# Kernel optimization log

Hardware: AMD Instinct MI355X
Metric: run time of the kernel (lower is better)

Reference implementation:

```python
import jax, jax.numpy as jnp
import numpy as np


def setup_inputs() -> dict:
    key = jax.random.key(0)
    C, S, NQ, H = 10, 10, 30, 1024  # n_classes, n_support, n_query, h_dim
    ks = jax.random.split(key, 6)
    x = jax.random.normal(ks[0], (C * (S + NQ), H), dtype=jnp.float32)
    # sorted, balanced labels so y.eq(c).nonzero() picks contiguous blocks
    y = jnp.repeat(jnp.arange(C, dtype=jnp.int32), S + NQ)
    W1 = jax.random.normal(ks[1], (H, H), dtype=jnp.float32) / np.sqrt(H)
    b1 = jnp.zeros((H,), dtype=jnp.float32)
    W2 = jax.random.normal(ks[2], (4 * H, H), dtype=jnp.float32) / np.sqrt(4 * H)
    b2 = jnp.zeros((H,), dtype=jnp.float32)
    return {"x": x, "W1": W1, "b1": b1, "W2": W2, "b2": b2,
            "y": y, "n_classes": C, "n_support": S, "n_query": NQ, "flag": 0}


def reference(x, W1, b1, W2, b2, y, n_classes, n_support, n_query, flag):
    # flag == 0 path; y is sorted & balanced, so the label-based gather in the
    # original (y.eq(c).nonzero()[:S] / [S:]) reduces to a reshape.
    C, S, NQ = n_classes, n_support, n_query
    H = x.shape[-1]
    xr = x.reshape(C, S + NQ, H)
    support = xr[:, :S]                      # [C, S, H]
    query = xr[:, S:].reshape(C * NQ, H)     # [Qt, H], Qt = C*NQ

    # fc1 computed ONCE on support/query, then broadcast (same math as
    # applying fc1 to the expanded tensors in the original).
    sf = jnp.einsum('csh,hd->csd', support, W1) + b1   # [C, S, H]
    qf = query @ W1 + b1                               # [Qt, H]

    # fc2 on concat([sf, qf, |sf-qf|, sf*qf]) split into 4 blocks of W2 so we
    # never materialize the [Qt, C, S, 4H] concat.
    Ws, Wq, Wc, Wd = W2[:H], W2[H:2 * H], W2[2 * H:3 * H], W2[3 * H:]
    a_s = jnp.einsum('csh,hd->csd', sf, Ws)            # [C, S, H]
    a_q = qf @ Wq                                      # [Qt, H]
    sfb = sf[None]                                     # [1, C, S, H]
    qfb = qf[:, None, None]                            # [Qt, 1, 1, H]
    d1 = jnp.abs(sfb - qfb)                            # [Qt, C, S, H]
    d2 = sfb * qfb                                     # [Qt, C, S, H]
    mca_ = (a_s[None] + a_q[:, None, None]
            + jnp.einsum('qcsh,hd->qcsd', d1, Wc)
            + jnp.einsum('qcsh,hd->qcsd', d2, Wd) + b2)  # [Qt, C, S, H]

    score = jax.nn.softmax(jnp.tanh(mca_).sum(-1), axis=-1)  # [Qt, C, S]
    proto = jnp.einsum('qcs,csh->qch', score, support)       # [Qt, C, H]
    dists = jnp.sum((proto - query[:, None, :]) ** 2, axis=-1)  # [Qt, C]
    return dists
```

## Files before the change

kernel.cpp:

```cpp
#include <hip/hip_runtime.h>
#include <hip/hip_bf16.h>
#include <math.h>

#define C_   10
#define S_   10
#define NQ_  30
#define H_   1024
#define Q_   300
#define ROWS_ 400

typedef __attribute__((ext_vector_type(8))) short s16x8;
typedef __attribute__((ext_vector_type(4))) float f32x4;

static __device__ __forceinline__ short f2b(float f) {
  __hip_bfloat16 h = __float2bfloat16(f);
  return __builtin_bit_cast(short, h);
}

static __device__ __forceinline__ float ftanh(float v) {
  v = fminf(fmaxf(v, -10.f), 10.f);
  float e = __expf(2.f * v);
  return (e - 1.f) / (e + 1.f);
}

__global__ __launch_bounds__(256) void feat_kernel(
    const float* __restrict__ x, const float* __restrict__ W1,
    const float* __restrict__ b1, float* __restrict__ f) {
  __shared__ float xs[4][H_];
  const int rt = blockIdx.x % 100;
  const int nt = blockIdx.x / 100;
  const int r0 = rt * 4;
  const int n0 = nt * 256;
  const int tid = threadIdx.x;

  for (int t = tid; t < 4 * H_ / 4; t += 256) {
    int r = t >> 8, h4 = (t & 255) * 4;
    *(float4*)&xs[r][h4] = *(const float4*)&x[(size_t)(r0 + r) * H_ + h4];
  }
  __syncthreads();

  float acc0 = 0.f, acc1 = 0.f, acc2 = 0.f, acc3 = 0.f;
  const float* __restrict__ wp = W1 + n0 + tid;
#pragma unroll 8
  for (int h = 0; h < H_; ++h) {
    float w = wp[(size_t)h * H_];
    acc0 = fmaf(xs[0][h], w, acc0);
    acc1 = fmaf(xs[1][h], w, acc1);
    acc2 = fmaf(xs[2][h], w, acc2);
    acc3 = fmaf(xs[3][h], w, acc3);
  }
  const int col = n0 + tid;
  const float bb = b1[col];
  f[(size_t)(r0 + 0) * H_ + col] = acc0 + bb;
  f[(size_t)(r0 + 1) * H_ + col] = acc1 + bb;
  f[(size_t)(r0 + 2) * H_ + col] = acc2 + bb;
  f[(size_t)(r0 + 3) * H_ + col] = acc3 + bb;
}

__global__ __launch_bounds__(256) void proj_kernel(
    const float* __restrict__ f, const float* __restrict__ W2,
    const float* __restrict__ b2, float* __restrict__ a) {
  __shared__ float fs[4][H_];
  const int rt = blockIdx.x % 100;
  const int nt = blockIdx.x / 100;
  const bool isSup = (rt < 25);
  const int i0 = isSup ? rt * 4 : (rt - 25) * 4;
  const int n0 = nt * 256;
  const float* __restrict__ W = isSup ? W2 : (W2 + (size_t)H_ * H_);
  const int tid = threadIdx.x;

  for (int t = tid; t < 4 * H_ / 4; t += 256) {
    int r = t >> 8, h4 = (t & 255) * 4;
    int i = i0 + r;
    int row = isSup ? ((i / 10) * 40 + (i % 10)) : ((i / 30) * 40 + 10 + (i % 30));
    *(float4*)&fs[r][h4] = *(const float4*)&f[(size_t)row * H_ + h4];
  }
  __syncthreads();

  float acc0 = 0.f, acc1 = 0.f, acc2 = 0.f, acc3 = 0.f;
  const float* __restrict__ wp = W + n0 + tid;
#pragma unroll 8
  for (int h = 0; h < H_; ++h) {
    float w = wp[(size_t)h * H_];
    acc0 = fmaf(fs[0][h], w, acc0);
    acc1 = fmaf(fs[1][h], w, acc1);
    acc2 = fmaf(fs[2][h], w, acc2);
    acc3 = fmaf(fs[3][h], w, acc3);
  }
  const int col = n0 + tid;
  const float bb = isSup ? 0.f : b2[col];
  const int o0 = isSup ? i0 : (100 + i0);
  a[(size_t)(o0 + 0) * H_ + col] = acc0 + bb;
  a[(size_t)(o0 + 1) * H_ + col] = acc1 + bb;
  a[(size_t)(o0 + 2) * H_ + col] = acc2 + bb;
  a[(size_t)(o0 + 3) * H_ + col] = acc3 + bb;
}

__global__ __launch_bounds__(256) void trans_kernel(
    const float* __restrict__ W2, unsigned short* __restrict__ Bt,
    float* __restrict__ logits) {
  const int b = blockIdx.x;
  const int tid = threadIdx.x;
  if (b == 512) {
    float4* lz = (float4*)logits;
    for (int i = tid; i < 7500; i += 256) lz[i] = make_float4(0.f, 0.f, 0.f, 0.f);
    return;
  }
  const int mat = b >> 8, kt = (b >> 4) & 15, ntl = b & 15;
  const float* __restrict__ src =
      W2 + (size_t)(2 + mat) * H_ * H_ + (size_t)(kt * 64) * H_ + ntl * 64;
  __shared__ float tl[64][65];
  {
    int r = tid >> 2, c4 = (tid & 3) * 16;
    const float* srcp = src + (size_t)r * H_ + c4;
#pragma unroll
    for (int j = 0; j < 4; ++j) {
      float4 v = *(const float4*)(srcp + j * 4);
      tl[r][c4 + j * 4 + 0] = v.x;
      tl[r][c4 + j * 4 + 1] = v.y;
      tl[r][c4 + j * 4 + 2] = v.z;
      tl[r][c4 + j * 4 + 3] = v.w;
    }
  }
  __syncthreads();
  {
    int n = tid >> 2, k0t = (tid & 3) * 16;
    s16x8 o0, o1;
#pragma unroll
    for (int j = 0; j < 8; ++j) {
      o0[j] = f2b(tl[k0t + j][n]);
      o1[j] = f2b(tl[k0t + 8 + j][n]);
    }
    unsigned short* dstp = Bt + (size_t)mat * H_ * H_ +
                           (size_t)(ntl * 64 + n) * H_ + kt * 64 + k0t;
    *(s16x8*)dstp = o0;
    *(s16x8*)(dstp + 8) = o1;
  }
}

__global__ __launch_bounds__(256, 2) void mca_mfma_kernel(
    const float* __restrict__ f, const float* __restrict__ a,
    const unsigned short* __restrict__ Bt, float* __restrict__ logits) {
  const int b = blockIdx.x;
  const int nt = b & 7;
  const int qt = (b >> 3) % 19;
  const int c = (b >> 3) / 19;
  const int q0 = qt * 16;
  const int n0 = nt * 128;

  __shared__ unsigned short Als[2][160 * 64];
  __shared__ unsigned short Bls[2][128 * 64];
  __shared__ float sl[2][26][36];

  const int tid = threadIdx.x;
  const int w = tid >> 6, lane = tid & 63;

  const int str = tid >> 3, sseg = tid & 7;
  int sgrow;
  if (str < 10) sgrow = c * 40 + str;
  else {
    int qg = q0 + (str - 10);
    if (qg > 299) qg = 299;
    sgrow = (qg / 30) * 40 + 10 + (qg % 30);
  }
  const float* fb_stage = f + (size_t)sgrow * H_ + sseg * 4;
  const unsigned st_off = (unsigned)(str * 144 + sseg * 16);

  const int rbase = tid >> 2, qtr = tid & 3;
  const bool has2 = (tid < 128);
  unsigned sboff[3], qboff[3], awx[3], aw2x[3];
#pragma unroll
  for (int j = 0; j < 3; ++j) {
    int row = (j < 2) ? (rbase + j * 64) : (128 + rbase);
    int qloc = row / 10, s = row - qloc * 10;
    sboff[j] = (unsigned)(s * 144 + qtr * 32);
    qboff[j] = (unsigned)((10 + qloc) * 144 + qtr * 32);
    unsigned asw = (unsigned)((row & 7) << 4);
    unsigned aw = (unsigned)(row * 128 + qtr * 16);
    awx[j] = aw ^ asw;
    aw2x[j] = (aw + 64) ^ asw;
  }

  const int rlo = lane >> 3;
  const int cch = (lane & 7) ^ rlo;
  const unsigned short* bsrc[4];
  unsigned bldso[4];
#pragma unroll
  for (int i = 0; i < 4; ++i) {
    int row = w * 32 + i * 8 + rlo;
    bsrc[i] = Bt + (size_t)(cch >> 2) * H_ * H_ + (size_t)(n0 + row) * H_ +
              (cch & 3) * 8;
    bldso[i] = (unsigned)(w * 4096 + i * 1024);
  }

  const int frow = lane & 15;
  const unsigned fkb = (unsigned)((lane >> 4) * 16);
  const unsigned swf = (unsigned)((frow & 7) << 4);
  const int wr = w >> 1, wc = w & 1;
  unsigned ard[5], brd[4];
#pragma unroll
  for (int m = 0; m < 5; ++m) ard[m] = (unsigned)((wr * 80 + m * 16 + frow) * 128);
#pragma unroll
  for (int nf = 0; nf < 4; ++nf) brd[nf] = (unsigned)((wc * 64 + nf * 16 + frow) * 128);

  f32x4 acc[5][4];
#pragma unroll
  for (int m = 0; m < 5; ++m)
#pragma unroll
    for (int nf = 0; nf < 4; ++nf) acc[m][nf] = (f32x4)(0.f);

#define STAGE(SLP, KS)                                                         \
  do {                                                                         \
    if (tid < 208) {                                                           \
      float4 v = *(const float4*)(fb_stage + (KS) * 32);                       \
      *(float4*)((char*)&sl[SLP][0][0] + st_off) = v;                          \
    }                                                                          \
  } while (0)

#define DMA_B(P, KG)                                                           \
  do {                                                                         \
    _Pragma("unroll") for (int i = 0; i < 4; ++i) {                            \
      __builtin_amdgcn_global_load_lds(                                        \
          (const __attribute__((address_space(1))) unsigned int*)(bsrc[i] + (KG)), \
          (__attribute__((address_space(3))) unsigned int*)((char*)&Bls[P][0] + bldso[i]), \
          16, 0, 0);                                                           \
    }                                                                          \
  } while (0)

#define GTASK(J, SLB, AB)                                                      \
  do {                                                                         \
    float4 sa = *(const float4*)((SLB) + sboff[J]);                            \
    float4 sb2 = *(const float4*)((SLB) + sboff[J] + 16);                      \
    float4 qa = *(const float4*)((SLB) + qboff[J]);                            \
    float4 qb2 = *(const float4*)((SLB) + qboff[J] + 16);                      \
    s16x8 d1, d2;                                                              \
    d1[0] = f2b(fabsf(sa.x - qa.x)); d2[0] = f2b(sa.x * qa.x);                 \
    d1[1] = f2b(fabsf(sa.y - qa.y)); d2[1] = f2b(sa.y * qa.y);                 \
    d1[2] = f2b(fabsf(sa.z - qa.z)); d2[2] = f2b(sa.z * qa.z);                 \
    d1[3] = f2b(fabsf(sa.w - qa.w)); d2[3] = f2b(sa.w * qa.w);                 \
    d1[4] = f2b(fabsf(sb2.x - qb2.x)); d2[4] = f2b(sb2.x * qb2.x);             \
    d1[5] = f2b(fabsf(sb2.y - qb2.y)); d2[5] = f2b(sb2.y * qb2.y);             \
    d1[6] = f2b(fabsf(sb2.z - qb2.z)); d2[6] = f2b(sb2.z * qb2.z);             \
    d1[7] = f2b(fabsf(sb2.w - qb2.w)); d2[7] = f2b(sb2.w * qb2.w);             \
    *(s16x8*)((AB) + awx[J]) = d1;                                             \
    *(s16x8*)((AB) + aw2x[J]) = d2;                                            \
  } while (0)

#define GENX(SLP, ABP)                                                         \
  do {                                                                         \
    const char* SLB = (const char*)&sl[SLP][0][0];                             \
    char* AB = (char*)&Als[ABP][0];                                            \
    GTASK(0, SLB, AB);                                                         \
    GTASK(1, SLB, AB);                                                         \
    if (has2) GTASK(2, SLB, AB);                                               \
  } while (0)

#define MFMA_PHASE(P)                                                          \
  do {                                                                         \
    const char* AB = (const char*)&Als[P][0];                                  \
    const char* BB = (const char*)&Bls[P][0];                                  \
    _Pragma("unroll") for (int kk = 0; kk < 2; ++kk) {                         \
      const unsigned kb = fkb + kk * 64;                                       \
      s16x8 bf0 = *(const s16x8*)(BB + ((brd[0] + kb) ^ swf));                 \
      s16x8 bf1 = *(const s16x8*)(BB + ((brd[1] + kb) ^ swf));                 \
      s16x8 bf2 = *(const s16x8*)(BB + ((brd[2] + kb) ^ swf));                 \
      s16x8 bf3 = *(const s16x8*)(BB + ((brd[3] + kb) ^ swf));                 \
      _Pragma("unroll") for (int m = 0; m < 5; ++m) {                          \
        s16x8 af = *(const s16x8*)(AB + ((ard[m] + kb) ^ swf));                \
        acc[m][0] = __builtin_amdgcn_mfma_f32_16x16x32_bf16(af, bf0, acc[m][0], 0, 0, 0); \
        acc[m][1] = __builtin_amdgcn_mfma_f32_16x16x32_bf16(af, bf1, acc[m][1], 0, 0, 0); \
        acc[m][2] = __builtin_amdgcn_mfma_f32_16x16x32_bf16(af, bf2, acc[m][2], 0, 0, 0); \
        acc[m][3] = __builtin_amdgcn_mfma_f32_16x16x32_bf16(af, bf3, acc[m][3], 0, 0, 0); \
      }                                                                        \
    }                                                                          \
  } while (0)

  STAGE(0, 0);
  STAGE(1, 1);
  DMA_B(0, 0);
  __syncthreads();
  GENX(0, 0);
  __syncthreads();

  for (int kp = 0; kp < 16; ++kp) {
    const int ks = kp * 2;
    DMA_B(1, (ks + 1) * 32);
    GENX(1, 1);
    __builtin_amdgcn_s_setprio(1);
    MFMA_PHASE(0);
    __builtin_amdgcn_s_setprio(0);
    if (kp < 15) STAGE(0, ks + 2);
    __syncthreads();

    if (kp < 15) {
      DMA_B(0, (ks + 2) * 32);
      GENX(0, 0);
      __builtin_amdgcn_s_setprio(1);
      MFMA_PHASE(1);
      __builtin_amdgcn_s_setprio(0);
      STAGE(1, ks + 3);
      __syncthreads();
    } else {
      __builtin_amdgcn_s_setprio(1);
      MFMA_PHASE(1);
      __builtin_amdgcn_s_setprio(0);
    }
  }

  const int colb = n0 + wc * 64 + frow;
  const int rgrp = (lane >> 4) * 4;
#pragma unroll
  for (int m = 0; m < 5; ++m) {
#pragma unroll
    for (int r = 0; r < 4; ++r) {
      const int row = wr * 80 + m * 16 + rgrp + r;
      const int qloc = row / 10, s = row - qloc * 10;
      const int q = q0 + qloc;
      float t = 0.f;
#pragma unroll
      for (int nf = 0; nf < 4; ++nf) {
        const int col = colb + nf * 16;
        float v = acc[m][nf][r] + a[(size_t)(c * 10 + s) * H_ + col] +
                  a[(size_t)(100 + q) * H_ + col];
        t += ftanh(v);
      }
      t += __shfl_xor(t, 1);
      t += __shfl_xor(t, 2);
      t += __shfl_xor(t, 4);
      t += __shfl_xor(t, 8);
      if ((lane & 15) == 0 && q < 300)
        atomicAdd(&logits[(q * 10 + c) * 10 + s], t);
    }
  }
#undef STAGE
#undef DMA_B
#undef GTASK
#undef GENX
#undef MFMA_PHASE
}

__global__ __launch_bounds__(256) void out_kernel(
    const float* __restrict__ x, const float* __restrict__ logits,
    float* __restrict__ dists) {
  const int q = blockIdx.x / 10;
  const int c = blockIdx.x % 10;
  const int tid = threadIdx.x;
  const int lane = tid & 63;
  const int wave = tid >> 6;
  __shared__ float red[4];

  float l[S_];
  float m = -1e30f;
#pragma unroll
  for (int s = 0; s < S_; ++s) {
    l[s] = logits[(q * 10 + c) * 10 + s];
    m = fmaxf(m, l[s]);
  }
  float sum = 0.f;
  float sc[S_];
#pragma unroll
  for (int s = 0; s < S_; ++s) {
    sc[s] = __expf(l[s] - m);
    sum += sc[s];
  }
  float inv = 1.f / sum;
#pragma unroll
  for (int s = 0; s < S_; ++s) sc[s] *= inv;

  const int qr = (q / 30) * 40 + 10 + (q % 30);
  float part = 0.f;
#pragma unroll
  for (int ii = 0; ii < 4; ++ii) {
    int i = tid + ii * 256;
    float p = 0.f;
#pragma unroll
    for (int s = 0; s < S_; ++s)
      p = fmaf(sc[s], x[(size_t)(c * 40 + s) * H_ + i], p);
    float d = p - x[(size_t)qr * H_ + i];
    part = fmaf(d, d, part);
  }
  for (int off = 32; off; off >>= 1) part += __shfl_down(part, off);
  if (lane == 0) red[wave] = part;
  __syncthreads();
  if (tid == 0) dists[q * 10 + c] = red[0] + red[1] + red[2] + red[3];
}

extern "C" void kernel_launch(void* const* d_in, const int* in_sizes, int n_in,
                              void* d_out, int out_size, void* d_ws, size_t ws_size,
                              hipStream_t stream) {
  const float* x = (const float*)d_in[0];
  const float* W1 = (const float*)d_in[1];
  const float* b1 = (const float*)d_in[2];
  const float* W2 = (const float*)d_in[3];
  const float* b2 = (const float*)d_in[4];
  float* out = (float*)d_out;

  float* f = (float*)d_ws;
  float* a = f + ROWS_ * H_;
  float* logits = a + ROWS_ * H_;
  unsigned short* Bt = (unsigned short*)(logits + 30208);

  feat_kernel<<<400, 256, 0, stream>>>(x, W1, b1, f);
  proj_kernel<<<400, 256, 0, stream>>>(f, W2, b2, a);
  trans_kernel<<<513, 256, 0, stream>>>(W2, Bt, logits);
  mca_mfma_kernel<<<10 * 19 * 8, 256, 0, stream>>>(f, a, Bt, logits);
  out_kernel<<<3000, 256, 0, stream>>>(x, logits, out);
}
```

Measured before the change: 316.3 us.

## Build MFMA A fragments in registers instead of staging through LDS

The mca kernel no longer writes the |s-q| and s*q bf16 tiles into a shared-memory A buffer. Each lane now computes its A fragments directly in registers from the staged fp32 support/query rows. The row mapping changes so each 16-row fragment is one support index across 16 queries. Dropping the A buffer frees about 40KB of LDS, and launch bounds move from 2 to 3 blocks per CU for more occupancy. In exchange, the elementwise/convert work is duplicated across the two column-waves, and the higher occupancy target may increase register pressure.

```diff
diff --git a/kernel.cpp b/kernel.cpp
--- a/kernel.cpp
+++ b/kernel.cpp
@@ -138,7 +138,7 @@
   }
 }
 
-__global__ __launch_bounds__(256, 2) void mca_mfma_kernel(
+__global__ __launch_bounds__(256, 3) void mca_mfma_kernel(
     const float* __restrict__ f, const float* __restrict__ a,
     const unsigned short* __restrict__ Bt, float* __restrict__ logits) {
   const int b = blockIdx.x;
@@ -148,12 +148,14 @@
   const int q0 = qt * 16;
   const int n0 = nt * 128;
 
-  __shared__ unsigned short Als[2][160 * 64];
   __shared__ unsigned short Bls[2][128 * 64];
   __shared__ float sl[2][26][36];
 
   const int tid = threadIdx.x;
   const int w = tid >> 6, lane = tid & 63;
+  const int frow = lane & 15;
+  const int lq = lane >> 4;
+  const int wr = w >> 1, wc = w & 1;
 
   const int str = tid >> 3, sseg = tid & 7;
   int sgrow;
@@ -166,20 +168,10 @@
   const float* fb_stage = f + (size_t)sgrow * H_ + sseg * 4;
   const unsigned st_off = (unsigned)(str * 144 + sseg * 16);
 
-  const int rbase = tid >> 2, qtr = tid & 3;
-  const bool has2 = (tid < 128);
-  unsigned sboff[3], qboff[3], awx[3], aw2x[3];
-#pragma unroll
-  for (int j = 0; j < 3; ++j) {
-    int row = (j < 2) ? (rbase + j * 64) : (128 + rbase);
-    int qloc = row / 10, s = row - qloc * 10;
-    sboff[j] = (unsigned)(s * 144 + qtr * 32);
-    qboff[j] = (unsigned)((10 + qloc) * 144 + qtr * 32);
-    unsigned asw = (unsigned)((row & 7) << 4);
-    unsigned aw = (unsigned)(row * 128 + qtr * 16);
-    awx[j] = aw ^ asw;
-    aw2x[j] = (aw + 64) ^ asw;
-  }
+  const unsigned qfo = (unsigned)((10 + frow) * 144 + lq * 32);
+  unsigned sfo[5];
+#pragma unroll
+  for (int m = 0; m < 5; ++m) sfo[m] = (unsigned)((wr * 5 + m) * 144 + lq * 32);
 
   const int rlo = lane >> 3;
   const int cch = (lane & 7) ^ rlo;
@@ -193,13 +185,9 @@
     bldso[i] = (unsigned)(w * 4096 + i * 1024);
   }
 
-  const int frow = lane & 15;
-  const unsigned fkb = (unsigned)((lane >> 4) * 16);
+  const unsigned fkb = (unsigned)(lq * 16);
   const unsigned swf = (unsigned)((frow & 7) << 4);
-  const int wr = w >> 1, wc = w & 1;
-  unsigned ard[5], brd[4];
-#pragma unroll
-  for (int m = 0; m < 5; ++m) ard[m] = (unsigned)((wr * 80 + m * 16 + frow) * 128);
+  unsigned brd[4];
 #pragma unroll
   for (int nf = 0; nf < 4; ++nf) brd[nf] = (unsigned)((wc * 64 + nf * 16 + frow) * 128);
 
@@ -227,101 +215,89 @@
     }                                                                          \
   } while (0)
 
-#define GTASK(J, SLB, AB)                                                      \
+#define STEP_BODY(P)                                                           \
   do {                                                                         \
-    float4 sa = *(const float4*)((SLB) + sboff[J]);                            \
-    float4 sb2 = *(const float4*)((SLB) + sboff[J] + 16);                      \
-    float4 qa = *(const float4*)((SLB) + qboff[J]);                            \
-    float4 qb2 = *(const float4*)((SLB) + qboff[J] + 16);                      \
-    s16x8 d1, d2;                                                              \
-    d1[0] = f2b(fabsf(sa.x - qa.x)); d2[0] = f2b(sa.x * qa.x);                 \
-    d1[1] = f2b(fabsf(sa.y - qa.y)); d2[1] = f2b(sa.y * qa.y);                 \
-    d1[2] = f2b(fabsf(sa.z - qa.z)); d2[2] = f2b(sa.z * qa.z);                 \
-    d1[3] = f2b(fabsf(sa.w - qa.w)); d2[3] = f2b(sa.w * qa.w);                 \
-    d1[4] = f2b(fabsf(sb2.x - qb2.x)); d2[4] = f2b(sb2.x * qb2.x);             \
-    d1[5] = f2b(fabsf(sb2.y - qb2.y)); d2[5] = f2b(sb2.y * qb2.y);             \
-    d1[6] = f2b(fabsf(sb2.z - qb2.z)); d2[6] = f2b(sb2.z * qb2.z);             \
-    d1[7] = f2b(fabsf(sb2.w - qb2.w)); d2[7] = f2b(sb2.w * qb2.w);             \
-    *(s16x8*)((AB) + awx[J]) = d1;                                             \
-    *(s16x8*)((AB) + aw2x[J]) = d2;                                            \
+    const char* SLB = (const char*)&sl[P][0][0];                               \
+    const char* BB = (const char*)&Bls[P][0];                                  \
+    float4 qa = *(const float4*)(SLB + qfo);                                   \
+    float4 qb = *(const float4*)(SLB + qfo + 16);                              \
+    s16x8 d1f[5], d2f[5];                                                      \
+    _Pragma("unroll") for (int m = 0; m < 5; ++m) {                            \
+      float4 sa = *(const float4*)(SLB + sfo[m]);                              \
+      float4 sb = *(const float4*)(SLB + sfo[m] + 16);                         \
+      s16x8 t1, t2;                                                            \
+      t1[0] = f2b(fabsf(sa.x - qa.x)); t2[0] = f2b(sa.x * qa.x);               \
+      t1[1] = f2b(fabsf(sa.y - qa.y)); t2[1] = f2b(sa.y * qa.y);               \
+      t1[2] = f2b(fabsf(sa.z - qa.z)); t2[2] = f2b(sa.z * qa.z);               \
+      t1[3] = f2b(fabsf(sa.w - qa.w)); t2[3] = f2b(sa.w * qa.w);               \
+      t1[4] = f2b(fabsf(sb.x - qb.x)); t2[4] = f2b(sb.x * qb.x);               \
+      t1[5] = f2b(fabsf(sb.y - qb.y)); t2[5] = f2b(sb.y * qb.y);               \
+      t1[6] = f2b(fabsf(sb.z - qb.z)); t2[6] = f2b(sb.z * qb.z);               \
+      t1[7] = f2b(fabsf(sb.w - qb.w)); t2[7] = f2b(sb.w * qb.w);               \
+      d1f[m] = t1; d2f[m] = t2;                                                \
+    }                                                                          \
+    __builtin_amdgcn_s_setprio(1);                                            \
+    {                                                                          \
+      s16x8 bf0 = *(const s16x8*)(BB + ((brd[0] + fkb) ^ swf));                \
+      s16x8 bf1 = *(const s16x8*)(BB + ((brd[1] + fkb) ^ swf));                \
+      s16x8 bf2 = *(const s16x8*)(BB + ((brd[2] + fkb) ^ swf));                \
+      s16x8 bf3 = *(const s16x8*)(BB + ((brd[3] + fkb) ^ swf));                \
+      _Pragma("unroll") for (int m = 0; m < 5; ++m) {                          \
+        acc[m][0] = __builtin_amdgcn_mfma_f32_16x16x32_bf16(d1f[m], bf0, acc[m][0], 0, 0, 0); \
+        acc[m][1] = __builtin_amdgcn_mfma_f32_16x16x32_bf16(d1f[m], bf1, acc[m][1], 0, 0, 0); \
+        acc[m][2] = __builtin_amdgcn_mfma_f32_16x16x32_bf16(d1f[m], bf2, acc[m][2], 0, 0, 0); \
+        acc[m][3] = __builtin_amdgcn_mfma_f32_16x16x32_bf16(d1f[m], bf3, acc[m][3], 0, 0, 0); \
+      }                                                                        \
+    }                                                                          \
+    {                                                                          \
+      s16x8 bf0 = *(const s16x8*)(BB + ((brd[0] + fkb + 64) ^ swf));           \
+      s16x8 bf1 = *(const s16x8*)(BB + ((brd[1] + fkb + 64) ^ swf));           \
+      s16x8 bf2 = *(const s16x8*)(BB + ((brd[2] + fkb + 64) ^ swf));           \
+      s16x8 bf3 = *(const s16x8*)(BB + ((brd[3] + fkb + 64) ^ swf));           \
+      _Pragma("unroll") for (int m = 0; m < 5; ++m) {                          \
+        acc[m][0] = __builtin_amdgcn_mfma_f32_16x16x32_bf16(d2f[m], bf0, acc[m][0], 0, 0, 0); \
+        acc[m][1] = __builtin_amdgcn_mfma_f32_16x16x32_bf16(d2f[m], bf1, acc[m][1], 0, 0, 0); \
+        acc[m][2] = __builtin_amdgcn_mfma_f32_16x16x32_bf16(d2f[m], bf2, acc[m][2], 0, 0, 0); \
+        acc[m][3] = __builtin_amdgcn_mfma_f32_16x16x32_bf16(d2f[m], bf3, acc[m][3], 0, 0, 0); \
+      }                                                                        \
+    }                                                                          \
+    __builtin_amdgcn_s_setprio(0);                                            \
   } while (0)
 
-#define GENX(SLP, ABP)                                                         \
-  do {                                                                         \
-    const char* SLB = (const char*)&sl[SLP][0][0];                             \
-    char* AB = (char*)&Als[ABP][0];                                            \
-    GTASK(0, SLB, AB);                                                         \
-    GTASK(1, SLB, AB);                                                         \
-    if (has2) GTASK(2, SLB, AB);                                               \
-  } while (0)
-
-#define MFMA_PHASE(P)                                                          \
-  do {                                                                         \
-    const char* AB = (const char*)&Als[P][0];                                  \
-    const char* BB = (const char*)&Bls[P][0];                                  \
-    _Pragma("unroll") for (int kk = 0; kk < 2; ++kk) {                         \
-      const unsigned kb = fkb + kk * 64;                                       \
-      s16x8 bf0 = *(const s16x8*)(BB + ((brd[0] + kb) ^ swf));                 \
-      s16x8 bf1 = *(const s16x8*)(BB + ((brd[1] + kb) ^ swf));                 \
-      s16x8 bf2 = *(const s16x8*)(BB + ((brd[2] + kb) ^ swf));                 \
-      s16x8 bf3 = *(const s16x8*)(BB + ((brd[3] + kb) ^ swf));                 \
-      _Pragma("unroll") for (int m = 0; m < 5; ++m) {                          \
-        s16x8 af = *(const s16x8*)(AB + ((ard[m] + kb) ^ swf));                \
-        acc[m][0] = __builtin_amdgcn_mfma_f32_16x16x32_bf16(af, bf0, acc[m][0], 0, 0, 0); \
-        acc[m][1] = __builtin_amdgcn_mfma_f32_16x16x32_bf16(af, bf1, acc[m][1], 0, 0, 0); \
-        acc[m][2] = __builtin_amdgcn_mfma_f32_16x16x32_bf16(af, bf2, acc[m][2], 0, 0, 0); \
-        acc[m][3] = __builtin_amdgcn_mfma_f32_16x16x32_bf16(af, bf3, acc[m][3], 0, 0, 0); \
-      }                                                                        \
-    }                                                                          \
-  } while (0)
-
   STAGE(0, 0);
-  STAGE(1, 1);
   DMA_B(0, 0);
-  __syncthreads();
-  GENX(0, 0);
   __syncthreads();
 
   for (int kp = 0; kp < 16; ++kp) {
     const int ks = kp * 2;
     DMA_B(1, (ks + 1) * 32);
-    GENX(1, 1);
-    __builtin_amdgcn_s_setprio(1);
-    MFMA_PHASE(0);
-    __builtin_amdgcn_s_setprio(0);
-    if (kp < 15) STAGE(0, ks + 2);
+    STAGE(1, ks + 1);
+    STEP_BODY(0);
     __syncthreads();
-
     if (kp < 15) {
       DMA_B(0, (ks + 2) * 32);
-      GENX(0, 0);
-      __builtin_amdgcn_s_setprio(1);
-      MFMA_PHASE(1);
-      __builtin_amdgcn_s_setprio(0);
-      STAGE(1, ks + 3);
+      STAGE(0, ks + 2);
+      STEP_BODY(1);
       __syncthreads();
     } else {
-      __builtin_amdgcn_s_setprio(1);
-      MFMA_PHASE(1);
-      __builtin_amdgcn_s_setprio(0);
+      STEP_BODY(1);
     }
   }
 
   const int colb = n0 + wc * 64 + frow;
-  const int rgrp = (lane >> 4) * 4;
+  const int rgrp = lq * 4;
 #pragma unroll
   for (int m = 0; m < 5; ++m) {
+    const int s = wr * 5 + m;
 #pragma unroll
     for (int r = 0; r < 4; ++r) {
-      const int row = wr * 80 + m * 16 + rgrp + r;
-      const int qloc = row / 10, s = row - qloc * 10;
-      const int q = q0 + qloc;
+      const int q = q0 + rgrp + r;
       float t = 0.f;
 #pragma unroll
       for (int nf = 0; nf < 4; ++nf) {
         const int col = colb + nf * 16;
         float v = acc[m][nf][r] + a[(size_t)(c * 10 + s) * H_ + col] +
-                  a[(size_t)(100 + q) * H_ + col];
+                  a[(size_t)(100 + (q < 300 ? q : 299)) * H_ + col];
         t += ftanh(v);
       }
       t += __shfl_xor(t, 1);
@@ -334,9 +310,7 @@
   }
 #undef STAGE
 #undef DMA_B
-#undef GTASK
-#undef GENX
-#undef MFMA_PHASE
+#undef STEP_BODY
 }
 
 __global__ __launch_bounds__(256) void out_kernel(
```

Measured after the change: 624.6 us. 1.98x slower.
